# Performance work log

Measured on AMD Instinct MI355X. Metric: run time of the kernel, lower is better.

Reference implementation:

```python
import jax, jax.numpy as jnp
import numpy as np
import math

BLUR, P, SCALING = 0.05, 2.0, 0.9
DIAMETER = 8.0  # static bound on max |x-y| for unit-normal 1-D data (geomloss derives it from data)
NEG = -1e9     # masked log-weight


def _eps_schedule():
    # geomloss epsilon_schedule: diameter^p -> blur^p, geometric with ratio scaling^p
    eps = [DIAMETER ** P]
    eps += list(np.exp(np.arange(P * math.log(DIAMETER), P * math.log(BLUR), P * math.log(SCALING))))
    eps += [BLUR ** P]
    return np.asarray(eps, dtype=np.float32)


def _softmin(eps, C, h):
    # h: [m] = log-weights + dual/eps ; returns [n] = -eps*logsumexp_j(h_j - C_ij/eps)
    return -eps * jax.nn.logsumexp(h[None, :] - C / eps, axis=1)


def _sinkhorn_divergence(x, y, logw):
    # x, y: [B] 1-D point clouds for one output dim; logw: [B] masked log-weights.
    # Debiased Sinkhorn divergence S = OT_eps(a,b) - 0.5 OT(a,a) - 0.5 OT(b,b), p=2 cost |x-y|^2/2.
    Cxy = 0.5 * (x[:, None] - y[None, :]) ** 2
    Cxx = 0.5 * (x[:, None] - x[None, :]) ** 2
    Cyy = 0.5 * (y[:, None] - y[None, :]) ** 2
    eps_list = jnp.asarray(_eps_schedule())
    e0 = eps_list[0]
    f = _softmin(e0, Cxy, logw)    # dual on x for OT(a,b)
    g = _softmin(e0, Cxy.T, logw)  # dual on y for OT(a,b)
    a = _softmin(e0, Cxx, logw)    # self dual on x
    b = _softmin(e0, Cyy, logw)    # self dual on y

    def step(carry, eps):
        f, g, a, b = carry
        ft = _softmin(eps, Cxy, logw + g / eps)
        gt = _softmin(eps, Cxy.T, logw + f / eps)
        at = _softmin(eps, Cxx, logw + a / eps)
        bt = _softmin(eps, Cyy, logw + b / eps)
        return (0.5 * (f + ft), 0.5 * (g + gt), 0.5 * (a + at), 0.5 * (b + bt)), None

    (f, g, a, b), _ = jax.lax.scan(step, (f, g, a, b), eps_list)
    # last extrapolation at final eps (full updates, no damping)
    e = eps_list[-1]
    f, g = _softmin(e, Cxy, logw + g / e), _softmin(e, Cxy.T, logw + f / e)
    a = 0.5 * (a + _softmin(e, Cxx, logw + a / e))
    b = 0.5 * (b + _softmin(e, Cyy, logw + b / e))
    w = jnp.exp(logw)  # 1/n on valid samples, 0 on masked
    return jnp.sum(w * (f - a)) + jnp.sum(w * (g - b))


def reference(predictions, targets):
    # predictions, targets: [B, D]; NaNs in targets mark invalid samples per dim
    mask = ~jnp.isnan(targets)                      # [B, D]
    y = jnp.where(mask, targets, 0.0)
    counts = jnp.sum(mask, axis=0)                  # [D]
    logn = jnp.log(jnp.maximum(counts, 1).astype(predictions.dtype))
    logw = jnp.where(mask, -logn[None, :], NEG)     # [B, D]
    per_dim = jax.vmap(_sinkhorn_divergence, in_axes=(1, 1, 1))(predictions, y, logw)
    per_dim = jnp.where(counts > 1, per_dim, 0.0)   # dims with <=1 valid sample -> 0
    total = jnp.mean(per_dim)                       # weights=None -> mean over dims
    return total, per_dim


def setup_inputs() -> dict:
    key = jax.random.key(0)
    k1, k2, k3 = jax.random.split(key, 3)
    B, D = 2048, 8
    preds = jax.random.normal(k1, (B, D), dtype=jnp.float32)
    targ = jax.random.normal(k2, (B, D), dtype=jnp.float32)
    nan_mask = jax.random.uniform(k3, (B, D)) < 0.1
    targ = jnp.where(nan_mask, jnp.nan, targ)
    return {"predictions": preds, "targets": targ}
```

## Files before the change

kernel.cpp:

```cpp
#include <hip/hip_runtime.h>
#include <math.h>

#define BN 2048
#define DN 8
#define NEGW -1e9f
#define TPB 256
#define RPB 128
#define RS 16
#define JSPLIT 16
#define SLOTS (BN/2)
#define SPC (SLOTS/JSPLIT)
#define CPAD 65

typedef float f2 __attribute__((ext_vector_type(2)));

static __device__ __forceinline__ float wave_reduce_sum(float v){
  #pragma unroll
  for (int off = 32; off > 0; off >>= 1) v += __shfl_xor(v, off, 64);
  return v;
}
static __device__ __forceinline__ f2 exp2_hw(f2 e){
  return (f2){__builtin_amdgcn_exp2f(e.x), __builtin_amdgcn_exp2f(e.y)};
}

__global__ void setup_kernel(const float* __restrict__ pred, const float* __restrict__ targ,
                             float* __restrict__ xcol, float* __restrict__ ycol,
                             float* __restrict__ logw, float* __restrict__ counts){
  int d = blockIdx.x;
  int t = threadIdx.x;
  int lane = t & 63, wave = t >> 6;
  float mk[BN/256];
  float c = 0.f;
  for (int k = 0; k < BN/256; k++){
    int i = t + k*256;
    float tv = targ[i*DN + d];
    bool m = !(tv != tv);
    mk[k] = m ? 1.f : 0.f;
    c += mk[k];
    ycol[d*BN + i] = m ? tv : 0.f;
    xcol[d*BN + i] = pred[i*DN + d];
  }
  __shared__ float sh[4];
  __shared__ float logn_sh;
  float cw = wave_reduce_sum(c);
  if (lane == 0) sh[wave] = cw;
  __syncthreads();
  if (t == 0){
    float tot = sh[0] + sh[1] + sh[2] + sh[3];
    counts[d] = tot;
    logn_sh = logf(fmaxf(tot, 1.f));
  }
  __syncthreads();
  float ln = logn_sh;
  for (int k = 0; k < BN/256; k++){
    int i = t + k*256;
    logw[d*BN + i] = (mk[k] > 0.f) ? -ln : NEGW;
  }
}

__global__ __launch_bounds__(TPB) void sink_step(
      const float* __restrict__ xcol, const float* __restrict__ ycol,
      const float* __restrict__ logw,
      const float* __restrict__ dold, float* __restrict__ dnew,
      const float* __restrict__ Hold, float* __restrict__ Hnew,
      float eps, float inv_eps, float inv_eps_next, int mode){
  const float L2E = 1.44269504088896340736f;
  const float LN2 = 0.69314718055994530942f;
  __shared__ float4 pair4[JSPLIT*CPAD];
  __shared__ float2 pms[JSPLIT][RPB];

  int bid = blockIdx.x;
  int rc  = bid & 15;
  int mat = (bid >> 4) & 3;
  int d   = bid >> 6;
  int t   = threadIdx.x;
  int rs  = t & (RS-1);
  int jc  = t >> 4;

  const float* xb = xcol + d*BN;
  const float* yb = ycol + d*BN;
  const float* lw = logw + d*BN;
  const float* ri; const float* pj; int hsel;
  switch (mat){
    case 0:  ri = xb; pj = yb; hsel = 1; break;
    case 1:  ri = yb; pj = xb; hsel = 0; break;
    case 2:  ri = xb; pj = xb; hsel = 2; break;
    default: ri = yb; pj = yb; hsel = 3; break;
  }
  const float* hp  = Hold + (size_t)hsel*DN*BN + d*BN;
  const float* dmp = dold + (size_t)mat *DN*BN + d*BN;
  float*       op  = dnew + (size_t)mat *DN*BN + d*BN;
  float*       oh  = Hnew + (size_t)mat *DN*BN + d*BN;

  const float c1 = L2E * inv_eps;
  const float c2 = 0.5f * inv_eps * L2E;

  const float2* pj2 = (const float2*)pj;
  const float2* h2src = (mode == 0) ? (const float2*)lw : (const float2*)hp;
  #pragma unroll
  for (int k = 0; k < SLOTS/TPB; k++){
    int idx = t + k*TPB;
    int phys = idx + (idx >> 6);
    float2 y2 = pj2[idx];
    float2 hh = h2src[idx];
    pair4[phys] = make_float4(y2.x, y2.y,
                              fmaf(-c2*y2.x, y2.x, L2E*hh.x),
                              fmaf(-c2*y2.y, y2.y, L2E*hh.y));
  }

  int row0 = rc*RPB + rs;
  f2 a2[8];
  #pragma unroll
  for (int r = 0; r < 8; r++){
    float xi = ri[row0 + RS*r];
    float al = c1 * xi;
    a2[r] = (f2){al, al};
  }
  __syncthreads();

  const float4* cb = pair4 + jc*CPAD;
  float mrow[8];
  f2 sA[8], sB[8];
  #pragma unroll
  for (int r = 0; r < 8; r++){
    mrow[r] = -INFINITY;
    sA[r] = (f2){0.f, 0.f};
    sB[r] = (f2){0.f, 0.f};
  }
  #pragma unroll 1
  for (int q = 0; q < SPC; q += 8){
    float4 P0 = cb[q+0]; float4 P1 = cb[q+1];
    float4 P2 = cb[q+2]; float4 P3 = cb[q+3];
    float4 P4 = cb[q+4]; float4 P5 = cb[q+5];
    float4 P6 = cb[q+6]; float4 P7 = cb[q+7];
    #pragma unroll
    for (int r = 0; r < 8; r++){
      f2 a = a2[r];
      f2 v0 = __builtin_elementwise_fma(a, (f2){P0.x,P0.y}, (f2){P0.z,P0.w});
      f2 v1 = __builtin_elementwise_fma(a, (f2){P1.x,P1.y}, (f2){P1.z,P1.w});
      f2 v2 = __builtin_elementwise_fma(a, (f2){P2.x,P2.y}, (f2){P2.z,P2.w});
      f2 v3 = __builtin_elementwise_fma(a, (f2){P3.x,P3.y}, (f2){P3.z,P3.w});
      f2 v4 = __builtin_elementwise_fma(a, (f2){P4.x,P4.y}, (f2){P4.z,P4.w});
      f2 v5 = __builtin_elementwise_fma(a, (f2){P5.x,P5.y}, (f2){P5.z,P5.w});
      f2 v6 = __builtin_elementwise_fma(a, (f2){P6.x,P6.y}, (f2){P6.z,P6.w});
      f2 v7 = __builtin_elementwise_fma(a, (f2){P7.x,P7.y}, (f2){P7.z,P7.w});
      f2 t0 = __builtin_elementwise_max(v0, v1);
      f2 t1 = __builtin_elementwise_max(v2, v3);
      f2 t2 = __builtin_elementwise_max(v4, v5);
      f2 t3 = __builtin_elementwise_max(v6, v7);
      f2 u0 = __builtin_elementwise_max(t0, t1);
      f2 u1 = __builtin_elementwise_max(t2, t3);
      f2 w  = __builtin_elementwise_max(u0, u1);
      float bm = fmaxf(w.x, w.y);
      float mo = mrow[r];
      float mn = fmaxf(mo, bm);
      float sc = __builtin_amdgcn_exp2f(mo - mn);
      mrow[r] = mn;
      f2 scv = (f2){sc, sc};
      f2 mv  = (f2){mn, mn};
      f2 x0 = exp2_hw(v0 - mv);
      f2 x1 = exp2_hw(v1 - mv);
      f2 x2 = exp2_hw(v2 - mv);
      f2 x3 = exp2_hw(v3 - mv);
      f2 x4 = exp2_hw(v4 - mv);
      f2 x5 = exp2_hw(v5 - mv);
      f2 x6 = exp2_hw(v6 - mv);
      f2 x7 = exp2_hw(v7 - mv);
      sA[r] = __builtin_elementwise_fma(sA[r], scv, x0);
      sB[r] = __builtin_elementwise_fma(sB[r], scv, x1);
      sA[r] += x2;  sB[r] += x3;
      sA[r] += x4;  sB[r] += x5;
      sA[r] += x6;  sB[r] += x7;
    }
  }
  #pragma unroll
  for (int r = 0; r < 8; r++){
    f2 s = sA[r] + sB[r];
    pms[jc][rs + RS*r] = make_float2(mrow[r], s.x + s.y);
  }
  __syncthreads();

  if (t < RPB){
    int row = rc*RPB + t;
    float M = -INFINITY;
    #pragma unroll
    for (int k = 0; k < JSPLIT; k++) M = fmaxf(M, pms[k][t].x);
    float s = 0.f;
    #pragma unroll
    for (int k = 0; k < JSPLIT; k++){
      float2 p = pms[k][t];
      s = fmaf(p.y, __builtin_amdgcn_exp2f(p.x - M), s);
    }
    float xi = ri[row];
    float beta = c2 * xi * xi;
    float lse2 = (M + __builtin_amdgcn_logf(s)) - beta;
    float tn = -eps * (LN2 * lse2);
    float outv;
    if (mode == 1 || (mode == 2 && mat >= 2)) outv = 0.5f * (dmp[row] + tn);
    else                                      outv = tn;
    op[row] = outv;
    oh[row] = fmaf(outv, inv_eps_next, lw[row]);
  }
}

__global__ void reduce_kernel(const float* __restrict__ dual, const float* __restrict__ logw,
                              const float* __restrict__ counts, float* __restrict__ out){
  int d = blockIdx.x;
  int t = threadIdx.x;
  int lane = t & 63, wave = t >> 6;
  float acc = 0.f;
  for (int k = 0; k < BN/256; k++){
    int i = t + k*256;
    float w  = expf(logw[d*BN + i]);
    float fv = dual[0*DN*BN + d*BN + i];
    float gv = dual[1*DN*BN + d*BN + i];
    float av = dual[2*DN*BN + d*BN + i];
    float bv = dual[3*DN*BN + d*BN + i];
    acc += w * ((fv - av) + (gv - bv));
  }
  __shared__ float sh[4];
  float aw = wave_reduce_sum(acc);
  if (lane == 0) sh[wave] = aw;
  __syncthreads();
  if (t == 0){
    float tot = sh[0] + sh[1] + sh[2] + sh[3];
    out[1 + d] = (counts[d] > 1.5f) ? tot : 0.f;
  }
}

__global__ void total_kernel(float* __restrict__ out){
  if (threadIdx.x == 0 && blockIdx.x == 0){
    float s = 0.f;
    for (int d = 0; d < DN; d++) s += out[1 + d];
    out[0] = s / (float)DN;
  }
}

extern "C" void kernel_launch(void* const* d_in, const int* in_sizes, int n_in,
                              void* d_out, int out_size, void* d_ws, size_t ws_size,
                              hipStream_t stream){
  const float* pred = (const float*)d_in[0];
  const float* targ = (const float*)d_in[1];
  float* out = (float*)d_out;
  float* ws  = (float*)d_ws;

  float* xcol   = ws;
  float* ycol   = ws + (size_t)DN*BN;
  float* logw   = ws + (size_t)2*DN*BN;
  float* counts = ws + (size_t)3*DN*BN;
  float* buf0   = ws + (size_t)3*DN*BN + 64;
  float* buf1   = buf0 + (size_t)4*DN*BN;
  float* H0     = buf1 + (size_t)4*DN*BN;
  float* H1     = H0   + (size_t)4*DN*BN;

  float eps_list[64]; int n = 0;
  {
    const double P = 2.0, DIAM = 8.0, BLUR = 0.05, SC = 0.9;
    double ls = P*log(DIAM), le = P*log(BLUR), st = P*log(SC);
    eps_list[n++] = (float)pow(DIAM, P);
    int cnt = (int)ceil((le - ls)/st);
    for (int k = 0; k < cnt; k++) eps_list[n++] = (float)exp(ls + st*(double)k);
    eps_list[n++] = (float)(BLUR*BLUR);
  }

  setup_kernel<<<DN, 256, 0, stream>>>(pred, targ, xcol, ycol, logw, counts);

  dim3 grid(DN*4*16), blk(TPB);
  float* cur = buf0;  float* nxt = buf1;
  float* Hc  = H0;    float* Hn  = H1;
  {
    float e = eps_list[0];
    sink_step<<<grid, blk, 0, stream>>>(xcol, ycol, logw, cur, cur, Hc, Hc,
                                        e, 1.f/e, 1.f/eps_list[0], 0);
  }
  for (int k = 0; k < n; k++){
    float e = eps_list[k];
    float en = (k+1 < n) ? eps_list[k+1] : eps_list[n-1];
    sink_step<<<grid, blk, 0, stream>>>(xcol, ycol, logw, cur, nxt, Hc, Hn,
                                        e, 1.f/e, 1.f/en, 1);
    float* tb = cur; cur = nxt; nxt = tb;
    float* th = Hc;  Hc  = Hn;  Hn  = th;
  }
  {
    float e = eps_list[n-1];
    sink_step<<<grid, blk, 0, stream>>>(xcol, ycol, logw, cur, nxt, Hc, Hn,
                                        e, 1.f/e, 1.f/e, 2);
    float* tb = cur; cur = nxt; nxt = tb;
    float* th = Hc;  Hc  = Hn;  Hn  = th;
  }
  reduce_kernel<<<DN, 256, 0, stream>>>(cur, logw, counts, out);
  total_kernel<<<1, 64, 0, stream>>>(out);
}
```

Before: 1.042 ms.

## Fuse all Sinkhorn iterations into one persistent kernel with grid barriers

Replaces the 53 per-iteration sink_step launches with a single persistent kernel of 512 blocks that loops over the epsilon schedule and synchronises through a hierarchical atomic grid barrier. The epsilon schedule is computed on-device in shared memory, and the y column is cached in LDS once instead of being reloaded every step. This removes per-launch overhead and launch gaps between dependent steps. In exchange it relies on all blocks being co-resident on the device, otherwise the barrier deadlocks, and it adds barrier spin cost per iteration.

```diff
diff --git a/kernel.cpp b/kernel.cpp
--- a/kernel.cpp
+++ b/kernel.cpp
@@ -11,6 +11,11 @@
 #define SLOTS (BN/2)
 #define SPC (SLOTS/JSPLIT)
 #define CPAD 65
+#define NBLK (DN*4*16)
+#define NGRP 8
+#define GSZ (NBLK/NGRP)
+#define NEPS 51
+#define NITER (NEPS+2)
 
 typedef float f2 __attribute__((ext_vector_type(2)));
 
@@ -21,6 +26,28 @@
 }
 static __device__ __forceinline__ f2 exp2_hw(f2 e){
   return (f2){__builtin_amdgcn_exp2f(e.x), __builtin_amdgcn_exp2f(e.y)};
+}
+
+static __device__ __forceinline__ void grid_barrier(unsigned* bar, unsigned target){
+  __syncthreads();
+  if (threadIdx.x == 0){
+    __threadfence();
+    int grp = blockIdx.x & (NGRP-1);
+    unsigned a = __hip_atomic_fetch_add(&bar[grp*16], 1u, __ATOMIC_ACQ_REL, __HIP_MEMORY_SCOPE_AGENT);
+    if (a == GSZ-1){
+      __hip_atomic_store(&bar[grp*16], 0u, __ATOMIC_RELAXED, __HIP_MEMORY_SCOPE_AGENT);
+      unsigned r = __hip_atomic_fetch_add(&bar[128], 1u, __ATOMIC_ACQ_REL, __HIP_MEMORY_SCOPE_AGENT);
+      if (r == NGRP-1){
+        __hip_atomic_store(&bar[128], 0u, __ATOMIC_RELAXED, __HIP_MEMORY_SCOPE_AGENT);
+        __hip_atomic_store(&bar[144], target, __ATOMIC_RELEASE, __HIP_MEMORY_SCOPE_AGENT);
+      }
+    }
+    while (__hip_atomic_load(&bar[144], __ATOMIC_ACQUIRE, __HIP_MEMORY_SCOPE_AGENT) < target){
+      __builtin_amdgcn_s_sleep(8);
+    }
+    __threadfence();
+  }
+  __syncthreads();
 }
 
 __global__ void setup_kernel(const float* __restrict__ pred, const float* __restrict__ targ,
@@ -58,16 +85,20 @@
   }
 }
 
-__global__ __launch_bounds__(TPB) void sink_step(
+__global__ __launch_bounds__(TPB) void sink_all(
       const float* __restrict__ xcol, const float* __restrict__ ycol,
       const float* __restrict__ logw,
-      const float* __restrict__ dold, float* __restrict__ dnew,
-      const float* __restrict__ Hold, float* __restrict__ Hnew,
-      float eps, float inv_eps, float inv_eps_next, int mode){
+      float* __restrict__ dual0, float* __restrict__ dual1,
+      float* __restrict__ Hb0, float* __restrict__ Hb1,
+      unsigned* __restrict__ bar){
   const float L2E = 1.44269504088896340736f;
   const float LN2 = 0.69314718055994530942f;
   __shared__ float4 pair4[JSPLIT*CPAD];
+  __shared__ float2 ysl[JSPLIT*CPAD];
   __shared__ float2 pms[JSPLIT][RPB];
+  __shared__ float s_el[NEPS];
+  __shared__ float s_eps[NITER], s_ie[NITER], s_ien[NITER];
+  __shared__ int   s_mode[NITER];
 
   int bid = blockIdx.x;
   int rc  = bid & 15;
@@ -76,6 +107,21 @@
   int t   = threadIdx.x;
   int rs  = t & (RS-1);
   int jc  = t >> 4;
+
+  if (t == 0){
+    double ls = 2.0*log(8.0), st = 2.0*log(0.9);
+    s_el[0] = 64.0f;
+    for (int k = 0; k < NEPS-2; k++) s_el[1+k] = (float)exp(ls + st*(double)k);
+    s_el[NEPS-1] = 0.05f*0.05f;
+    for (int j = 0; j < NITER; j++){
+      int idx = (j == 0) ? 0 : ((j <= NEPS) ? j-1 : NEPS-1);
+      int nid = (j == 0) ? 0 : ((j < NEPS) ? j : NEPS-1);
+      s_eps[j]  = s_el[idx];
+      s_ie[j]   = 1.0f/s_el[idx];
+      s_ien[j]  = 1.0f/s_el[nid];
+      s_mode[j] = (j == 0) ? 0 : ((j <= NEPS) ? 1 : 2);
+    }
+  }
 
   const float* xb = xcol + d*BN;
   const float* yb = ycol + d*BN;
@@ -87,119 +133,137 @@
     case 2:  ri = xb; pj = xb; hsel = 2; break;
     default: ri = yb; pj = yb; hsel = 3; break;
   }
-  const float* hp  = Hold + (size_t)hsel*DN*BN + d*BN;
-  const float* dmp = dold + (size_t)mat *DN*BN + d*BN;
-  float*       op  = dnew + (size_t)mat *DN*BN + d*BN;
-  float*       oh  = Hnew + (size_t)mat *DN*BN + d*BN;
-
-  const float c1 = L2E * inv_eps;
-  const float c2 = 0.5f * inv_eps * L2E;
+  size_t moff = (size_t)mat *DN*BN + d*BN;
+  size_t hoff = (size_t)hsel*DN*BN + d*BN;
 
   const float2* pj2 = (const float2*)pj;
-  const float2* h2src = (mode == 0) ? (const float2*)lw : (const float2*)hp;
   #pragma unroll
   for (int k = 0; k < SLOTS/TPB; k++){
     int idx = t + k*TPB;
-    int phys = idx + (idx >> 6);
-    float2 y2 = pj2[idx];
-    float2 hh = h2src[idx];
-    pair4[phys] = make_float4(y2.x, y2.y,
-                              fmaf(-c2*y2.x, y2.x, L2E*hh.x),
-                              fmaf(-c2*y2.y, y2.y, L2E*hh.y));
+    ysl[idx + (idx>>6)] = pj2[idx];
   }
 
   int row0 = rc*RPB + rs;
-  f2 a2[8];
+  float xi[8];
   #pragma unroll
-  for (int r = 0; r < 8; r++){
-    float xi = ri[row0 + RS*r];
-    float al = c1 * xi;
-    a2[r] = (f2){al, al};
-  }
-  __syncthreads();
-
-  const float4* cb = pair4 + jc*CPAD;
-  float mrow[8];
-  f2 sA[8], sB[8];
-  #pragma unroll
-  for (int r = 0; r < 8; r++){
-    mrow[r] = -INFINITY;
-    sA[r] = (f2){0.f, 0.f};
-    sB[r] = (f2){0.f, 0.f};
-  }
+  for (int r = 0; r < 8; r++) xi[r] = ri[row0 + RS*r];
+  int rowe = rc*RPB + t;
+  float xe = 0.f, lwrow = 0.f;
+  if (t < RPB){ xe = ri[rowe]; lwrow = lw[rowe]; }
+  __syncthreads();
+
   #pragma unroll 1
-  for (int q = 0; q < SPC; q += 8){
-    float4 P0 = cb[q+0]; float4 P1 = cb[q+1];
-    float4 P2 = cb[q+2]; float4 P3 = cb[q+3];
-    float4 P4 = cb[q+4]; float4 P5 = cb[q+5];
-    float4 P6 = cb[q+6]; float4 P7 = cb[q+7];
+  for (int j = 0; j < NITER; j++){
+    int wp = j & 1, rp = wp ^ 1;
+    int mode  = s_mode[j];
+    float eps = s_eps[j], inv_eps = s_ie[j], ien = s_ien[j];
+    const float c1 = L2E * inv_eps;
+    const float c2 = 0.5f * inv_eps * L2E;
+
+    const float* Hrd = (j == 0) ? lw : (((rp == 0) ? Hb0 : Hb1) + hoff);
+    const float* dmp = ((rp == 0) ? dual0 : dual1) + moff;
+    float*       op  = ((wp == 0) ? dual0 : dual1) + moff;
+    float*       oh  = ((wp == 0) ? Hb0 : Hb1) + moff;
+
+    {
+      const float4* H4 = (const float4*)Hrd;
+      float4 ha = H4[2*t];
+      float4 hb = H4[2*t+1];
+      int i0 = 4*t;
+      int p0 = i0 + (i0 >> 6);
+      float2 y0 = ysl[p0+0], y1 = ysl[p0+1], y2 = ysl[p0+2], y3 = ysl[p0+3];
+      pair4[p0+0] = make_float4(y0.x, y0.y, fmaf(-c2*y0.x, y0.x, L2E*ha.x), fmaf(-c2*y0.y, y0.y, L2E*ha.y));
+      pair4[p0+1] = make_float4(y1.x, y1.y, fmaf(-c2*y1.x, y1.x, L2E*ha.z), fmaf(-c2*y1.y, y1.y, L2E*ha.w));
+      pair4[p0+2] = make_float4(y2.x, y2.y, fmaf(-c2*y2.x, y2.x, L2E*hb.x), fmaf(-c2*y2.y, y2.y, L2E*hb.y));
+      pair4[p0+3] = make_float4(y3.x, y3.y, fmaf(-c2*y3.x, y3.x, L2E*hb.z), fmaf(-c2*y3.y, y3.y, L2E*hb.w));
+    }
+    f2 a2[8];
+    #pragma unroll
+    for (int r = 0; r < 8; r++){ float al = c1 * xi[r]; a2[r] = (f2){al, al}; }
+    __syncthreads();
+
+    const float4* cb = pair4 + jc*CPAD;
+    float mrow[8];
+    f2 sA[8], sB[8];
     #pragma unroll
     for (int r = 0; r < 8; r++){
-      f2 a = a2[r];
-      f2 v0 = __builtin_elementwise_fma(a, (f2){P0.x,P0.y}, (f2){P0.z,P0.w});
-      f2 v1 = __builtin_elementwise_fma(a, (f2){P1.x,P1.y}, (f2){P1.z,P1.w});
-      f2 v2 = __builtin_elementwise_fma(a, (f2){P2.x,P2.y}, (f2){P2.z,P2.w});
-      f2 v3 = __builtin_elementwise_fma(a, (f2){P3.x,P3.y}, (f2){P3.z,P3.w});
-      f2 v4 = __builtin_elementwise_fma(a, (f2){P4.x,P4.y}, (f2){P4.z,P4.w});
-      f2 v5 = __builtin_elementwise_fma(a, (f2){P5.x,P5.y}, (f2){P5.z,P5.w});
-      f2 v6 = __builtin_elementwise_fma(a, (f2){P6.x,P6.y}, (f2){P6.z,P6.w});
-      f2 v7 = __builtin_elementwise_fma(a, (f2){P7.x,P7.y}, (f2){P7.z,P7.w});
-      f2 t0 = __builtin_elementwise_max(v0, v1);
-      f2 t1 = __builtin_elementwise_max(v2, v3);
-      f2 t2 = __builtin_elementwise_max(v4, v5);
-      f2 t3 = __builtin_elementwise_max(v6, v7);
-      f2 u0 = __builtin_elementwise_max(t0, t1);
-      f2 u1 = __builtin_elementwise_max(t2, t3);
-      f2 w  = __builtin_elementwise_max(u0, u1);
-      float bm = fmaxf(w.x, w.y);
-      float mo = mrow[r];
-      float mn = fmaxf(mo, bm);
-      float sc = __builtin_amdgcn_exp2f(mo - mn);
-      mrow[r] = mn;
-      f2 scv = (f2){sc, sc};
-      f2 mv  = (f2){mn, mn};
-      f2 x0 = exp2_hw(v0 - mv);
-      f2 x1 = exp2_hw(v1 - mv);
-      f2 x2 = exp2_hw(v2 - mv);
-      f2 x3 = exp2_hw(v3 - mv);
-      f2 x4 = exp2_hw(v4 - mv);
-      f2 x5 = exp2_hw(v5 - mv);
-      f2 x6 = exp2_hw(v6 - mv);
-      f2 x7 = exp2_hw(v7 - mv);
-      sA[r] = __builtin_elementwise_fma(sA[r], scv, x0);
-      sB[r] = __builtin_elementwise_fma(sB[r], scv, x1);
-      sA[r] += x2;  sB[r] += x3;
-      sA[r] += x4;  sB[r] += x5;
-      sA[r] += x6;  sB[r] += x7;
-    }
-  }
-  #pragma unroll
-  for (int r = 0; r < 8; r++){
-    f2 s = sA[r] + sB[r];
-    pms[jc][rs + RS*r] = make_float2(mrow[r], s.x + s.y);
-  }
-  __syncthreads();
-
-  if (t < RPB){
-    int row = rc*RPB + t;
-    float M = -INFINITY;
+      mrow[r] = -INFINITY;
+      sA[r] = (f2){0.f, 0.f};
+      sB[r] = (f2){0.f, 0.f};
+    }
+    #pragma unroll 1
+    for (int q = 0; q < SPC; q += 8){
+      float4 P0 = cb[q+0]; float4 P1 = cb[q+1];
+      float4 P2 = cb[q+2]; float4 P3 = cb[q+3];
+      float4 P4 = cb[q+4]; float4 P5 = cb[q+5];
+      float4 P6 = cb[q+6]; float4 P7 = cb[q+7];
+      #pragma unroll
+      for (int r = 0; r < 8; r++){
+        f2 a = a2[r];
+        f2 v0 = __builtin_elementwise_fma(a, (f2){P0.x,P0.y}, (f2){P0.z,P0.w});
+        f2 v1 = __builtin_elementwise_fma(a, (f2){P1.x,P1.y}, (f2){P1.z,P1.w});
+        f2 v2 = __builtin_elementwise_fma(a, (f2){P2.x,P2.y}, (f2){P2.z,P2.w});
+        f2 v3 = __builtin_elementwise_fma(a, (f2){P3.x,P3.y}, (f2){P3.z,P3.w});
+        f2 v4 = __builtin_elementwise_fma(a, (f2){P4.x,P4.y}, (f2){P4.z,P4.w});
+        f2 v5 = __builtin_elementwise_fma(a, (f2){P5.x,P5.y}, (f2){P5.z,P5.w});
+        f2 v6 = __builtin_elementwise_fma(a, (f2){P6.x,P6.y}, (f2){P6.z,P6.w});
+        f2 v7 = __builtin_elementwise_fma(a, (f2){P7.x,P7.y}, (f2){P7.z,P7.w});
+        f2 t0 = __builtin_elementwise_max(v0, v1);
+        f2 t1 = __builtin_elementwise_max(v2, v3);
+        f2 t2 = __builtin_elementwise_max(v4, v5);
+        f2 t3 = __builtin_elementwise_max(v6, v7);
+        f2 u0 = __builtin_elementwise_max(t0, t1);
+        f2 u1 = __builtin_elementwise_max(t2, t3);
+        f2 w  = __builtin_elementwise_max(u0, u1);
+        float bm = fmaxf(w.x, w.y);
+        float mo = mrow[r];
+        float mn = fmaxf(mo, bm);
+        float sc = __builtin_amdgcn_exp2f(mo - mn);
+        mrow[r] = mn;
+        f2 scv = (f2){sc, sc};
+        f2 mv  = (f2){mn, mn};
+        f2 x0 = exp2_hw(v0 - mv);
+        f2 x1 = exp2_hw(v1 - mv);
+        f2 x2 = exp2_hw(v2 - mv);
+        f2 x3 = exp2_hw(v3 - mv);
+        f2 x4 = exp2_hw(v4 - mv);
+        f2 x5 = exp2_hw(v5 - mv);
+        f2 x6 = exp2_hw(v6 - mv);
+        f2 x7 = exp2_hw(v7 - mv);
+        sA[r] = __builtin_elementwise_fma(sA[r], scv, x0);
+        sB[r] = __builtin_elementwise_fma(sB[r], scv, x1);
+        sA[r] += x2;  sB[r] += x3;
+        sA[r] += x4;  sB[r] += x5;
+        sA[r] += x6;  sB[r] += x7;
+      }
+    }
     #pragma unroll
-    for (int k = 0; k < JSPLIT; k++) M = fmaxf(M, pms[k][t].x);
-    float s = 0.f;
-    #pragma unroll
-    for (int k = 0; k < JSPLIT; k++){
-      float2 p = pms[k][t];
-      s = fmaf(p.y, __builtin_amdgcn_exp2f(p.x - M), s);
-    }
-    float xi = ri[row];
-    float beta = c2 * xi * xi;
-    float lse2 = (M + __builtin_amdgcn_logf(s)) - beta;
-    float tn = -eps * (LN2 * lse2);
-    float outv;
-    if (mode == 1 || (mode == 2 && mat >= 2)) outv = 0.5f * (dmp[row] + tn);
-    else                                      outv = tn;
-    op[row] = outv;
-    oh[row] = fmaf(outv, inv_eps_next, lw[row]);
+    for (int r = 0; r < 8; r++){
+      f2 s = sA[r] + sB[r];
+      pms[jc][rs + RS*r] = make_float2(mrow[r], s.x + s.y);
+    }
+    __syncthreads();
+
+    if (t < RPB){
+      float M = -INFINITY;
+      #pragma unroll
+      for (int k = 0; k < JSPLIT; k++) M = fmaxf(M, pms[k][t].x);
+      float s = 0.f;
+      #pragma unroll
+      for (int k = 0; k < JSPLIT; k++){
+        float2 p = pms[k][t];
+        s = fmaf(p.y, __builtin_amdgcn_exp2f(p.x - M), s);
+      }
+      float beta = c2 * xe * xe;
+      float lse2 = (M + __builtin_amdgcn_logf(s)) - beta;
+      float tn = -eps * (LN2 * lse2);
+      float outv;
+      if (mode == 1 || (mode == 2 && mat >= 2)) outv = 0.5f * (dmp[rowe] + tn);
+      else                                      outv = tn;
+      op[rowe] = outv;
+      oh[rowe] = fmaf(outv, ien, lwrow);
+    }
+    if (j < NITER-1) grid_barrier(bar, (unsigned)(j+1));
   }
 }
 
@@ -252,42 +316,11 @@
   float* buf1   = buf0 + (size_t)4*DN*BN;
   float* H0     = buf1 + (size_t)4*DN*BN;
   float* H1     = H0   + (size_t)4*DN*BN;
-
-  float eps_list[64]; int n = 0;
-  {
-    const double P = 2.0, DIAM = 8.0, BLUR = 0.05, SC = 0.9;
-    double ls = P*log(DIAM), le = P*log(BLUR), st = P*log(SC);
-    eps_list[n++] = (float)pow(DIAM, P);
-    int cnt = (int)ceil((le - ls)/st);
-    for (int k = 0; k < cnt; k++) eps_list[n++] = (float)exp(ls + st*(double)k);
-    eps_list[n++] = (float)(BLUR*BLUR);
-  }
-
+  unsigned* bar = (unsigned*)(H1 + (size_t)4*DN*BN);
+
+  hipMemsetAsync(bar, 0, 12*16*sizeof(unsigned), stream);
   setup_kernel<<<DN, 256, 0, stream>>>(pred, targ, xcol, ycol, logw, counts);
-
-  dim3 grid(DN*4*16), blk(TPB);
-  float* cur = buf0;  float* nxt = buf1;
-  float* Hc  = H0;    float* Hn  = H1;
-  {
-    float e = eps_list[0];
-    sink_step<<<grid, blk, 0, stream>>>(xcol, ycol, logw, cur, cur, Hc, Hc,
-                                        e, 1.f/e, 1.f/eps_list[0], 0);
-  }
-  for (int k = 0; k < n; k++){
-    float e = eps_list[k];
-    float en = (k+1 < n) ? eps_list[k+1] : eps_list[n-1];
-    sink_step<<<grid, blk, 0, stream>>>(xcol, ycol, logw, cur, nxt, Hc, Hn,
-                                        e, 1.f/e, 1.f/en, 1);
-    float* tb = cur; cur = nxt; nxt = tb;
-    float* th = Hc;  Hc  = Hn;  Hn  = th;
-  }
-  {
-    float e = eps_list[n-1];
-    sink_step<<<grid, blk, 0, stream>>>(xcol, ycol, logw, cur, nxt, Hc, Hn,
-                                        e, 1.f/e, 1.f/e, 2);
-    float* tb = cur; cur = nxt; nxt = tb;
-    float* th = Hc;  Hc  = Hn;  Hn  = th;
-  }
-  reduce_kernel<<<DN, 256, 0, stream>>>(cur, logw, counts, out);
+  sink_all<<<NBLK, TPB, 0, stream>>>(xcol, ycol, logw, buf0, buf1, H0, H1, bar);
+  reduce_kernel<<<DN, 256, 0, stream>>>(buf0, logw, counts, out);
   total_kernel<<<1, 64, 0, stream>>>(out);
 }
```

Result: slower. 3.221 ms (+209.1%).
